# Performance work log

Measured on AMD Instinct MI355X. Metric: run time of the kernel, lower is better.

Reference implementation:

```python
import jax, jax.numpy as jnp
import numpy as np

OLD = (32, 32)   # fine grid coord_dims
NEW = (16, 16)   # coarse grid (dims // 2)
N_ORDERS = 6     # multi-indices of total order <= 2 in 2 coords


def lin_resize(x, new_size, axis):
    # 1D linear interpolation along `axis`, align_corners=True (matches F.interpolate)
    old = x.shape[axis]
    pos = jnp.arange(new_size, dtype=x.dtype) * ((old - 1) / (new_size - 1))
    lo = jnp.clip(jnp.floor(pos).astype(jnp.int32), 0, old - 2)
    w = pos - lo.astype(x.dtype)
    xl = jnp.take(x, lo, axis=axis)
    xh = jnp.take(x, lo + 1, axis=axis)
    shp = [1] * x.ndim
    shp[axis] = new_size
    w = w.reshape(shp)
    return xl * (1.0 - w) + xh * w


def bilinear_resize(x, new_hw):
    # separable bilinear, align_corners=True; x is [..., H, W]
    x = lin_resize(x, new_hw[0], x.ndim - 2)
    return lin_resize(x, new_hw[1], x.ndim - 1)


def setup_inputs():
    key = jax.random.key(0)
    ks = jax.random.split(key, 6)
    B = 32                      # bs * n_ind_dim = 8 * 4
    G = OLD[0] * OLD[1]         # fine grid size = 1024
    m, n = 2048, 1536           # coarse constraints x coarse vars (16*16*6)
    return {
        "coeffs": jax.random.normal(ks[0], (B, G, N_ORDERS), jnp.float32),
        "rhs": jax.random.normal(ks[1], (B, G), jnp.float32),
        "steps_x": jax.random.uniform(ks[2], (B, OLD[0] - 1), jnp.float32),
        "steps_y": jax.random.uniform(ks[3], (B, OLD[1] - 1), jnp.float32),
        "A": jax.random.normal(ks[4], (B, m, n), jnp.float32) * 0.05,
        "A_rhs": jax.random.normal(ks[5], (B, m), jnp.float32),
    }


def reference(coeffs, rhs, steps_x, steps_y, A, A_rhs):
    B = coeffs.shape[0]
    new_G = NEW[0] * NEW[1]

    # --- downsample_coeffs: [B,G,O] -> [B,O,H,W] -> bilinear -> [B,newG,O]
    c = coeffs.transpose(0, 2, 1).reshape(B, N_ORDERS, OLD[0], OLD[1])
    c = bilinear_resize(c, NEW)
    new_coeffs = c.reshape(B, N_ORDERS, new_G).transpose(0, 2, 1)

    # --- downsample_rhs: [B,G] -> [B,1,H,W] -> bilinear -> [B,newG]
    r = bilinear_resize(rhs.reshape(B, 1, OLD[0], OLD[1]), NEW)
    new_rhs = r.reshape(B, new_G)

    # --- downsample_steps: drop last, pairwise sum
    nsx = steps_x[:, :-1].reshape(B, OLD[0] // 2 - 1, 2).sum(axis=-1)
    nsy = steps_y[:, :-1].reshape(B, OLD[1] // 2 - 1, 2).sum(axis=-1)

    # --- make_AtA (coarsest path: dense bmm) ---
    AtA = jnp.einsum('bmn,bmk->bnk', A, A)           # At @ A, [B,n,n]
    AtPrhs = jnp.einsum('bmn,bm->bn', A, A_rhs)      # At @ rhs
    D = jnp.sum(A * A, axis=1)                       # diag(AtA) = column sums of squares

    # --- L/U split (get_tril): L = cols <= rows, U = cols > rows ---
    n = AtA.shape[-1]
    ridx = jnp.arange(n)
    lmask = ridx[:, None] >= ridx[None, :]
    L = jnp.where(lmask, AtA, jnp.zeros((), AtA.dtype))
    U = jnp.where(lmask, jnp.zeros((), AtA.dtype), AtA)

    return (new_coeffs, new_rhs, nsx, nsy, AtA, AtPrhs, D, L, U)
```

## Files before the change

### kernel.cpp

```cpp
#include <hip/hip_runtime.h>
#include <math.h>

#define NB 32
#define M 2048
#define N 1536
#define NORD 6

#define OFF_COEFFS 0
#define OFF_RHS    49152
#define OFF_NSX    57344
#define OFF_NSY    57824
#define OFF_ATA    58304
#define OFF_ATPRHS 75555776
#define OFF_D      75604928
#define OFF_L      75654080
#define OFF_U      151151552
#define SMALL_TOTAL 58304

typedef short short8v __attribute__((ext_vector_type(8)));
typedef float f32x4 __attribute__((ext_vector_type(4)));

__device__ __forceinline__ void gload16(const void* g, void* l) {
    __builtin_amdgcn_global_load_lds(
        (const __attribute__((address_space(1))) void*)g,
        (__attribute__((address_space(3))) void*)l, 16, 0, 0);
}

__device__ __forceinline__ uint rtn_bf16(float x) {
    uint u = __float_as_uint(x);
    return (u + 0x7fffu + ((u >> 16) & 1u)) >> 16;
}

__device__ __forceinline__ void nts(float v, float* p) {
    __builtin_nontemporal_store(v, p);
}
__device__ __forceinline__ void nts4(f32x4 v, float* p) {
    __builtin_nontemporal_store(v, (f32x4*)p);
}

__global__ void small_kernel(const float* __restrict__ coeffs,
                             const float* __restrict__ rhs,
                             const float* __restrict__ sx,
                             const float* __restrict__ sy,
                             float* __restrict__ out) {
    int idx = blockIdx.x * blockDim.x + threadIdx.x;
    if (idx >= SMALL_TOTAL) return;
    const float scale = 31.0f / 15.0f;
    if (idx < 49152) {
        int b = idx / 1536;
        int rem = idx % 1536;
        int gp = rem / 6;
        int o  = rem % 6;
        int yy = gp / 16, xx = gp % 16;
        float py = (float)yy * scale;
        int ly = (int)floorf(py); if (ly > 30) ly = 30;
        float wy = py - (float)ly;
        float px = (float)xx * scale;
        int lx = (int)floorf(px); if (lx > 30) lx = 30;
        float wx = px - (float)lx;
        const float* base = coeffs + (size_t)b * 1024 * NORD;
        float v00 = base[(ly * 32 + lx) * NORD + o];
        float v01 = base[(ly * 32 + lx + 1) * NORD + o];
        float v10 = base[((ly + 1) * 32 + lx) * NORD + o];
        float v11 = base[((ly + 1) * 32 + lx + 1) * NORD + o];
        float a  = v00 * (1.0f - wy) + v10 * wy;
        float bb = v01 * (1.0f - wy) + v11 * wy;
        out[OFF_COEFFS + idx] = a * (1.0f - wx) + bb * wx;
    } else if (idx < 57344) {
        int j = idx - 49152;
        int b = j / 256;
        int gp = j % 256;
        int yy = gp / 16, xx = gp % 16;
        float py = (float)yy * scale;
        int ly = (int)floorf(py); if (ly > 30) ly = 30;
        float wy = py - (float)ly;
        float px = (float)xx * scale;
        int lx = (int)floorf(px); if (lx > 30) lx = 30;
        float wx = px - (float)lx;
        const float* base = rhs + (size_t)b * 1024;
        float v00 = base[ly * 32 + lx];
        float v01 = base[ly * 32 + lx + 1];
        float v10 = base[(ly + 1) * 32 + lx];
        float v11 = base[(ly + 1) * 32 + lx + 1];
        float a  = v00 * (1.0f - wy) + v10 * wy;
        float bb = v01 * (1.0f - wy) + v11 * wy;
        out[OFF_RHS + j] = a * (1.0f - wx) + bb * wx;
    } else if (idx < 57824) {
        int j = idx - 57344;
        int b = j / 15, k = j % 15;
        out[OFF_NSX + j] = sx[b * 31 + 2 * k] + sx[b * 31 + 2 * k + 1];
    } else {
        int j = idx - 57824;
        int b = j / 15, k = j % 15;
        out[OFF_NSY + j] = sy[b * 31 + 2 * k] + sy[b * 31 + 2 * k + 1];
    }
}

__global__ __launch_bounds__(256) void split_kernel(const float* __restrict__ A,
                                                    const float* __restrict__ Arhs,
                                                    ushort* __restrict__ Ahi,
                                                    float2* __restrict__ part) {
    int bid = blockIdx.x;
    int q  = bid & 3;
    int cb = (bid >> 2) % 6;
    int b  = bid / 24;
    int t  = threadIdx.x;
    int col = cb * 256 + t;
    const float* Ab = A + (size_t)b * M * N;
    const float* rb = Arhs + (size_t)b * M;
    uint4* Hp = (uint4*)Ahi;
    float s1 = 0.0f, s2 = 0.0f;
    for (int oct = q * 64; oct < q * 64 + 64; ++oct) {
        uint hw[4];
#pragma unroll
        for (int j = 0; j < 4; ++j) {
            float a0 = Ab[(size_t)(oct * 8 + 2 * j) * N + col];
            float a1 = Ab[(size_t)(oct * 8 + 2 * j + 1) * N + col];
            float r0 = rb[oct * 8 + 2 * j];
            float r1 = rb[oct * 8 + 2 * j + 1];
            s1 = fmaf(a0, r0, s1); s1 = fmaf(a1, r1, s1);
            s2 = fmaf(a0, a0, s2); s2 = fmaf(a1, a1, s2);
            hw[j] = rtn_bf16(a0) | (rtn_bf16(a1) << 16);
        }
        Hp[(size_t)(b * 256 + oct) * N + col] = make_uint4(hw[0], hw[1], hw[2], hw[3]);
    }
    part[(size_t)q * (NB * 6 * 256) + (size_t)(b * 6 + cb) * 256 + t] = make_float2(s1, s2);
}

__global__ __launch_bounds__(256) void reduce_kernel(const float2* __restrict__ part,
                                                     float* __restrict__ out) {
    int idx = blockIdx.x * 256 + threadIdx.x;
    float s1 = 0.0f, s2 = 0.0f;
#pragma unroll
    for (int q = 0; q < 4; ++q) {
        float2 p = part[(size_t)q * (NB * 6 * 256) + idx];
        s1 += p.x; s2 += p.y;
    }
    out[OFF_ATPRHS + idx] = s1;
    out[OFF_D + idx] = s2;
}

#define SYRK_BLOCKS (NB * 42)

__global__ __launch_bounds__(512, 4) void syrk1_kernel(const ushort* __restrict__ Ahi,
                                                       float* __restrict__ out) {
    __shared__ ushort lds[2][1536 * 8];

    int bid = blockIdx.x;
    int swz = (bid % 8) * (SYRK_BLOCKS / 8) + bid / 8;
    int b  = swz / 42;
    int p2 = swz % 42;
    int p = p2 >> 1, half = p2 & 1;
    int ti = 0;
    while ((ti + 1) * (ti + 2) / 2 <= p) ++ti;
    int tj = p - ti * (ti + 1) / 2;
    bool diag = (ti == tj);
    int i0 = ti * 256;
    int j0 = tj * 256 + half * 128;

    int t = threadIdx.x, w = t >> 6, l = t & 63;
    int wr = w >> 1, wc = w & 1;
    int lc = l & 15, lg = l >> 4;

    const ushort* base = Ahi + (size_t)b * 256 * N * 8;

    f32x4 acc[4][4];
#pragma unroll
    for (int i = 0; i < 4; ++i)
#pragma unroll
        for (int j = 0; j < 4; ++j)
#pragma unroll
            for (int k = 0; k < 4; ++k) acc[i][j][k] = 0.0f;

    auto stage = [&](int buf, int s) {
#pragma unroll
        for (int q = 0; q < 2; ++q) {
            int g0 = q * 512 + w * 64;
            int oct = (g0 >> 8) & 3, col0 = g0 & 255;
            gload16(base + ((size_t)(s * 4 + oct) * N + i0 + col0 + l) * 8,
                    &lds[buf][(oct * 256 + col0) * 8]);
        }
        {
            int oct = w >> 1, col0 = (w & 1) * 64;
            gload16(base + ((size_t)(s * 4 + oct) * N + j0 + col0 + l) * 8,
                    &lds[buf][1024 * 8 + (oct * 128 + col0) * 8]);
        }
    };

    int cur = 0;
    stage(0, 0);

    for (int s = 0; s < 64; ++s) {
        if (s < 63) {
            stage(cur ^ 1, s + 1);
            asm volatile("s_waitcnt vmcnt(3)" ::: "memory");
        } else {
            asm volatile("s_waitcnt vmcnt(0)" ::: "memory");
        }
        __builtin_amdgcn_s_barrier();
        asm volatile("" ::: "memory");

        short8v Bv[4];
#pragma unroll
        for (int bj = 0; bj < 4; ++bj) {
            int cp = wc * 64 + bj * 16 + lc;
            Bv[bj] = *(const short8v*)&lds[cur][1024 * 8 + (lg * 128 + cp) * 8];
        }
        __builtin_amdgcn_s_setprio(1);
#pragma unroll
        for (int ai = 0; ai < 4; ++ai) {
            short8v Av = *(const short8v*)&lds[cur][(lg * 256 + wr * 64 + ai * 16 + lc) * 8];
#pragma unroll
            for (int bj = 0; bj < 4; ++bj)
                acc[ai][bj] = __builtin_amdgcn_mfma_f32_16x16x32_bf16(Av, Bv[bj], acc[ai][bj], 0, 0, 0);
        }
        __builtin_amdgcn_s_setprio(0);

        asm volatile("" ::: "memory");
        __builtin_amdgcn_s_barrier();
        cur ^= 1;
    }

    float* AtA = out + OFF_ATA + (size_t)b * N * N;
    float* Lo  = out + OFF_L   + (size_t)b * N * N;
    float* Up  = out + OFF_U   + (size_t)b * N * N;

#pragma unroll
    for (int ai = 0; ai < 4; ++ai) {
        int gi0 = i0 + wr * 64 + ai * 16 + lg * 4;
#pragma unroll
        for (int bj = 0; bj < 4; ++bj) {
            int gj = j0 + wc * 64 + bj * 16 + lc;
#pragma unroll
            for (int r = 0; r < 4; ++r) {
                int gi = gi0 + r;
                float v = acc[ai][bj][r];
                size_t o = (size_t)gi * N + gj;
                nts(v, AtA + o);
                nts((gj <= gi) ? v : 0.0f, Lo + o);
                nts((gj >  gi) ? v : 0.0f, Up + o);
            }
            if (!diag) {
                f32x4 va = acc[ai][bj], vl, vu;
#pragma unroll
                for (int r = 0; r < 4; ++r) {
                    int gi = gi0 + r;
                    vl[r] = (gi <= gj) ? va[r] : 0.0f;
                    vu[r] = (gi >  gj) ? va[r] : 0.0f;
                }
                size_t om = (size_t)gj * N + gi0;
                nts4(va, AtA + om);
                nts4(vl, Lo  + om);
                nts4(vu, Up  + om);
            }
        }
    }
}

__global__ __launch_bounds__(256) void atp_d_kernel(const float* __restrict__ A,
                                                    const float* __restrict__ Arhs,
                                                    float* __restrict__ out) {
    int b  = blockIdx.x / 6;
    int cb = blockIdx.x % 6;
    int col = cb * 256 + threadIdx.x;
    const float* Ab = A + (size_t)b * M * N;
    const float* rb = Arhs + (size_t)b * M;
    float s1 = 0.0f, s2 = 0.0f;
#pragma unroll 4
    for (int m = 0; m < M; ++m) {
        float a = Ab[(size_t)m * N + col];
        float r = rb[m];
        s1 = fmaf(a, r, s1);
        s2 = fmaf(a, a, s2);
    }
    out[OFF_ATPRHS + b * N + col] = s1;
    out[OFF_D      + b * N + col] = s2;
}

#define BM 128
#define BK 16
#define NPAIRS 78

__global__ __launch_bounds__(256, 2) void syrk_kernel(const float* __restrict__ A,
                                                      float* __restrict__ out) {
    __shared__ float As[BK][BM];
    __shared__ float Bs[BK][BM];

    int bid = blockIdx.x;
    int b = bid / NPAIRS;
    int p = bid % NPAIRS;
    int ti = (int)((sqrtf(8.0f * (float)p + 1.0f) - 1.0f) * 0.5f);
    while ((ti + 1) * (ti + 2) / 2 <= p) ++ti;
    while (ti * (ti + 1) / 2 > p) --ti;
    int tj = p - ti * (ti + 1) / 2;
    int i0 = ti * BM, j0 = tj * BM;

    const float* Ab = A + (size_t)b * M * N;
    int t = threadIdx.x;
    int tx = t % 16, ty = t / 16;
    int lcv = (t % 32) * 4;
    int lk = t / 32;

    float acc[2][4][2][4] = {};

    for (int m0 = 0; m0 < M; m0 += BK) {
        const float* pa = Ab + (size_t)(m0 + lk) * N;
        float4 a0 = *(const float4*)(pa + i0 + lcv);
        float4 a1 = *(const float4*)(pa + (size_t)8 * N + i0 + lcv);
        float4 b0 = *(const float4*)(pa + j0 + lcv);
        float4 b1 = *(const float4*)(pa + (size_t)8 * N + j0 + lcv);
        *(float4*)&As[lk][lcv]     = a0;
        *(float4*)&As[lk + 8][lcv] = a1;
        *(float4*)&Bs[lk][lcv]     = b0;
        *(float4*)&Bs[lk + 8][lcv] = b1;
        __syncthreads();
#pragma unroll
        for (int kk = 0; kk < BK; ++kk) {
            float ar[2][4], br[2][4];
            *(float4*)&ar[0][0] = *(const float4*)&As[kk][ty * 4];
            *(float4*)&ar[1][0] = *(const float4*)&As[kk][64 + ty * 4];
            *(float4*)&br[0][0] = *(const float4*)&Bs[kk][tx * 4];
            *(float4*)&br[1][0] = *(const float4*)&Bs[kk][64 + tx * 4];
#pragma unroll
            for (int rh = 0; rh < 2; ++rh)
#pragma unroll
                for (int r = 0; r < 4; ++r)
#pragma unroll
                    for (int ch = 0; ch < 2; ++ch)
#pragma unroll
                        for (int c = 0; c < 4; ++c)
                            acc[rh][r][ch][c] = fmaf(ar[rh][r], br[ch][c], acc[rh][r][ch][c]);
        }
        __syncthreads();
    }

    float* AtA = out + OFF_ATA + (size_t)b * N * N;
    float* L   = out + OFF_L   + (size_t)b * N * N;
    float* U   = out + OFF_U   + (size_t)b * N * N;

#pragma unroll
    for (int rh = 0; rh < 2; ++rh)
#pragma unroll
        for (int r = 0; r < 4; ++r) {
            int gi = i0 + rh * 64 + ty * 4 + r;
#pragma unroll
            for (int ch = 0; ch < 2; ++ch) {
                int gjb = j0 + ch * 64 + tx * 4;
                float ta[4], tl[4], tu[4];
#pragma unroll
                for (int c = 0; c < 4; ++c) {
                    int gj = gjb + c;
                    float v = acc[rh][r][ch][c];
                    ta[c] = v;
                    tl[c] = (gj <= gi) ? v : 0.0f;
                    tu[c] = (gj >  gi) ? v : 0.0f;
                }
                size_t o = (size_t)gi * N + gjb;
                *(float4*)(AtA + o) = *(float4*)ta;
                *(float4*)(L   + o) = *(float4*)tl;
                *(float4*)(U   + o) = *(float4*)tu;
            }
        }

    if (ti != tj) {
#pragma unroll
        for (int ch = 0; ch < 2; ++ch)
#pragma unroll
            for (int c = 0; c < 4; ++c) {
                int gj = j0 + ch * 64 + tx * 4 + c;
#pragma unroll
                for (int rh = 0; rh < 2; ++rh) {
                    int gib = i0 + rh * 64 + ty * 4;
                    float ta[4], tl[4], tu[4];
#pragma unroll
                    for (int r = 0; r < 4; ++r) {
                        int gi = gib + r;
                        float v = acc[rh][r][ch][c];
                        ta[r] = v;
                        tl[r] = (gi <= gj) ? v : 0.0f;
                        tu[r] = (gi >  gj) ? v : 0.0f;
                    }
                    size_t o = (size_t)gj * N + gib;
                    *(float4*)(AtA + o) = *(float4*)ta;
                    *(float4*)(L   + o) = *(float4*)tl;
                    *(float4*)(U   + o) = *(float4*)tu;
                }
            }
    }
}

extern "C" void kernel_launch(void* const* d_in, const int* in_sizes, int n_in,
                              void* d_out, int out_size, void* d_ws, size_t ws_size,
                              hipStream_t stream) {
    const float* coeffs = (const float*)d_in[0];
    const float* rhs    = (const float*)d_in[1];
    const float* sx     = (const float*)d_in[2];
    const float* sy     = (const float*)d_in[3];
    const float* A      = (const float*)d_in[4];
    const float* Arhs   = (const float*)d_in[5];
    float* out = (float*)d_out;

    small_kernel<<<(SMALL_TOTAL + 255) / 256, 256, 0, stream>>>(coeffs, rhs, sx, sy, out);

    const size_t hi_bytes   = (size_t)NB * M * N * sizeof(ushort);
    const size_t part_bytes = (size_t)4 * NB * 6 * 256 * sizeof(float2);
    if (ws_size >= hi_bytes + part_bytes) {
        ushort* Ahi  = (ushort*)d_ws;
        float2* part = (float2*)((char*)d_ws + hi_bytes);
        split_kernel<<<768, 256, 0, stream>>>(A, Arhs, Ahi, part);
        reduce_kernel<<<192, 256, 0, stream>>>(part, out);
        syrk1_kernel<<<SYRK_BLOCKS, 512, 0, stream>>>(Ahi, out);
    } else {
        atp_d_kernel<<<NB * 6, 256, 0, stream>>>(A, Arhs, out);
        syrk_kernel<<<NB * NPAIRS, 256, 0, stream>>>(A, out);
    }
}
```

Before: 519.8 us.

## Use 256x256 SYRK tiles with deeper multi-stage LDS pipeline

```diff
diff --git a/kernel.cpp b/kernel.cpp
--- a/kernel.cpp
+++ b/kernel.cpp
@@ -140,85 +140,108 @@
     out[OFF_D + idx] = s2;
 }
 
-#define SYRK_BLOCKS (NB * 42)
-
-__global__ __launch_bounds__(512, 4) void syrk1_kernel(const ushort* __restrict__ Ahi,
+#define SYRK8_BLOCKS (NB * 21)
+
+__global__ __launch_bounds__(512, 2) void syrk8_kernel(const ushort* __restrict__ Ahi,
                                                        float* __restrict__ out) {
-    __shared__ ushort lds[2][1536 * 8];
+    __shared__ ushort lds[2][2][8 * 256 * 8];
 
     int bid = blockIdx.x;
-    int swz = (bid % 8) * (SYRK_BLOCKS / 8) + bid / 8;
-    int b  = swz / 42;
-    int p2 = swz % 42;
-    int p = p2 >> 1, half = p2 & 1;
+    int swz = (bid % 8) * (SYRK8_BLOCKS / 8) + bid / 8;
+    int b  = swz / 21;
+    int pp = swz % 21;
     int ti = 0;
-    while ((ti + 1) * (ti + 2) / 2 <= p) ++ti;
-    int tj = p - ti * (ti + 1) / 2;
+    while ((ti + 1) * (ti + 2) / 2 <= pp) ++ti;
+    int tj = pp - ti * (ti + 1) / 2;
     bool diag = (ti == tj);
-    int i0 = ti * 256;
-    int j0 = tj * 256 + half * 128;
+    int i0 = ti * 256, j0 = tj * 256;
 
     int t = threadIdx.x, w = t >> 6, l = t & 63;
-    int wr = w >> 1, wc = w & 1;
+    int wr = w >> 2, wc = w & 3;
     int lc = l & 15, lg = l >> 4;
 
     const ushort* base = Ahi + (size_t)b * 256 * N * 8;
 
-    f32x4 acc[4][4];
-#pragma unroll
-    for (int i = 0; i < 4; ++i)
+    f32x4 acc[8][4];
+#pragma unroll
+    for (int i = 0; i < 8; ++i)
 #pragma unroll
         for (int j = 0; j < 4; ++j)
 #pragma unroll
             for (int k = 0; k < 4; ++k) acc[i][j][k] = 0.0f;
 
-    auto stage = [&](int buf, int s) {
-#pragma unroll
-        for (int q = 0; q < 2; ++q) {
-            int g0 = q * 512 + w * 64;
-            int oct = (g0 >> 8) & 3, col0 = g0 & 255;
-            gload16(base + ((size_t)(s * 4 + oct) * N + i0 + col0 + l) * 8,
-                    &lds[buf][(oct * 256 + col0) * 8]);
-        }
-        {
-            int oct = w >> 1, col0 = (w & 1) * 64;
-            gload16(base + ((size_t)(s * 4 + oct) * N + j0 + col0 + l) * 8,
-                    &lds[buf][1024 * 8 + (oct * 128 + col0) * 8]);
+    int oc0 = t >> 8;
+    int scol = t & 255;
+    auto stage_unit = [&](int n) {
+        int kt = n >> 2, u = n & 3;
+        int arr = u & 1, h = u >> 1;
+        int colb = arr ? j0 : i0;
+        ushort* reg = &lds[kt & 1][arr][0];
+#pragma unroll
+        for (int c = 0; c < 2; ++c) {
+            int oct = h * 4 + c * 2 + oc0;
+            gload16(base + ((size_t)(kt * 8 + oct) * N + colb + scol) * 8,
+                    reg + (size_t)(oct * 256 + scol) * 8);
         }
     };
 
-    int cur = 0;
-    stage(0, 0);
-
-    for (int s = 0; s < 64; ++s) {
-        if (s < 63) {
-            stage(cur ^ 1, s + 1);
-            asm volatile("s_waitcnt vmcnt(3)" ::: "memory");
-        } else {
-            asm volatile("s_waitcnt vmcnt(0)" ::: "memory");
-        }
-        __builtin_amdgcn_s_barrier();
-        asm volatile("" ::: "memory");
-
+    for (int n = 0; n < 8; ++n) stage_unit(n);
+    asm volatile("s_waitcnt vmcnt(12)" ::: "memory");
+    __builtin_amdgcn_s_barrier();
+
+    for (int it = 0; it < 16; ++it) {
         short8v Bv[4];
 #pragma unroll
-        for (int bj = 0; bj < 4; ++bj) {
-            int cp = wc * 64 + bj * 16 + lc;
-            Bv[bj] = *(const short8v*)&lds[cur][1024 * 8 + (lg * 128 + cp) * 8];
-        }
-        __builtin_amdgcn_s_setprio(1);
-#pragma unroll
-        for (int ai = 0; ai < 4; ++ai) {
-            short8v Av = *(const short8v*)&lds[cur][(lg * 256 + wr * 64 + ai * 16 + lc) * 8];
-#pragma unroll
-            for (int bj = 0; bj < 4; ++bj)
-                acc[ai][bj] = __builtin_amdgcn_mfma_f32_16x16x32_bf16(Av, Bv[bj], acc[ai][bj], 0, 0, 0);
-        }
-        __builtin_amdgcn_s_setprio(0);
-
-        asm volatile("" ::: "memory");
-        __builtin_amdgcn_s_barrier();
-        cur ^= 1;
+        for (int p = 0; p < 8; ++p) {
+            const int buf  = p >> 2;
+            const int ksub = (p >> 1) & 1;
+            const int ch   = p & 1;
+            const ushort* Areg = &lds[buf][0][0];
+            const ushort* Breg = &lds[buf][1][0];
+
+            short8v Av[4];
+#pragma unroll
+            for (int aif = 0; aif < 4; ++aif) {
+                int ai = ch * 4 + aif;
+                Av[aif] = *(const short8v*)
+                    &Areg[(size_t)((ksub * 4 + lg) * 256 + wr * 128 + ai * 16 + lc) * 8];
+            }
+            if (ch == 0) {
+#pragma unroll
+                for (int bj = 0; bj < 4; ++bj)
+                    Bv[bj] = *(const short8v*)
+                        &Breg[(size_t)((ksub * 4 + lg) * 256 + wc * 64 + bj * 16 + lc) * 8];
+            }
+
+            int g = it * 8 + p;
+            if (g >= 2 && g <= 121) stage_unit(g + 6);
+
+            asm volatile("" ::: "memory");
+            __builtin_amdgcn_s_barrier();
+            asm volatile("s_waitcnt lgkmcnt(0)" ::: "memory");
+            __builtin_amdgcn_sched_barrier(0);
+
+            __builtin_amdgcn_s_setprio(1);
+#pragma unroll
+            for (int aif = 0; aif < 4; ++aif)
+#pragma unroll
+                for (int bj = 0; bj < 4; ++bj)
+                    acc[ch * 4 + aif][bj] = __builtin_amdgcn_mfma_f32_16x16x32_bf16(
+                        Av[aif], Bv[bj], acc[ch * 4 + aif][bj], 0, 0, 0);
+            __builtin_amdgcn_s_setprio(0);
+
+            if (p == 1) {
+                if (it == 15) asm volatile("s_waitcnt vmcnt(4)" ::: "memory");
+                else          asm volatile("s_waitcnt vmcnt(8)" ::: "memory");
+            } else if (p == 3 || p == 5) {
+                if (it == 15) asm volatile("s_waitcnt vmcnt(0)" ::: "memory");
+                else          asm volatile("s_waitcnt vmcnt(8)" ::: "memory");
+            } else if (p == 7) {
+                if (it != 15) asm volatile("s_waitcnt vmcnt(8)" ::: "memory");
+            }
+            asm volatile("" ::: "memory");
+            __builtin_amdgcn_s_barrier();
+        }
     }
 
     float* AtA = out + OFF_ATA + (size_t)b * N * N;
@@ -226,8 +249,8 @@
     float* Up  = out + OFF_U   + (size_t)b * N * N;
 
 #pragma unroll
-    for (int ai = 0; ai < 4; ++ai) {
-        int gi0 = i0 + wr * 64 + ai * 16 + lg * 4;
+    for (int ai = 0; ai < 8; ++ai) {
+        int gi0 = i0 + wr * 128 + ai * 16 + lg * 4;
 #pragma unroll
         for (int bj = 0; bj < 4; ++bj) {
             int gj = j0 + wc * 64 + bj * 16 + lc;
@@ -409,7 +432,7 @@
         float2* part = (float2*)((char*)d_ws + hi_bytes);
         split_kernel<<<768, 256, 0, stream>>>(A, Arhs, Ahi, part);
         reduce_kernel<<<192, 256, 0, stream>>>(part, out);
-        syrk1_kernel<<<SYRK_BLOCKS, 512, 0, stream>>>(Ahi, out);
+        syrk8_kernel<<<SYRK8_BLOCKS, 512, 0, stream>>>(Ahi, out);
     } else {
         atp_d_kernel<<<NB * 6, 256, 0, stream>>>(A, Arhs, out);
         syrk_kernel<<<NB * NPAIRS, 256, 0, stream>>>(A, out);
```

Result: slower. 531.9 us (+2.3%).

## Use 128x128 SYRK tiles with 256-thread blocks and shared diagonal operand

Applied to the files above, without the earlier changes.

```diff
diff --git a/kernel.cpp b/kernel.cpp
--- a/kernel.cpp
+++ b/kernel.cpp
@@ -140,23 +140,21 @@
     out[OFF_D + idx] = s2;
 }
 
-#define SYRK_BLOCKS (NB * 42)
-
-__global__ __launch_bounds__(512, 4) void syrk1_kernel(const ushort* __restrict__ Ahi,
+#define SYRK_BLOCKS (NB * 78)
+
+__global__ __launch_bounds__(256, 4) void syrk3_kernel(const ushort* __restrict__ Ahi,
                                                        float* __restrict__ out) {
-    __shared__ ushort lds[2][1536 * 8];
+    __shared__ ushort lds[2][1024 * 8];
 
     int bid = blockIdx.x;
     int swz = (bid % 8) * (SYRK_BLOCKS / 8) + bid / 8;
-    int b  = swz / 42;
-    int p2 = swz % 42;
-    int p = p2 >> 1, half = p2 & 1;
+    int b = swz / 78;
+    int p = swz % 78;
     int ti = 0;
     while ((ti + 1) * (ti + 2) / 2 <= p) ++ti;
     int tj = p - ti * (ti + 1) / 2;
     bool diag = (ti == tj);
-    int i0 = ti * 256;
-    int j0 = tj * 256 + half * 128;
+    int i0 = ti * 128, j0 = tj * 128;
 
     int t = threadIdx.x, w = t >> 6, l = t & 63;
     int wr = w >> 1, wc = w & 1;
@@ -172,44 +170,45 @@
 #pragma unroll
             for (int k = 0; k < 4; ++k) acc[i][j][k] = 0.0f;
 
+    int nq = diag ? 2 : 4;
     auto stage = [&](int buf, int s) {
-#pragma unroll
-        for (int q = 0; q < 2; ++q) {
-            int g0 = q * 512 + w * 64;
-            int oct = (g0 >> 8) & 3, col0 = g0 & 255;
-            gload16(base + ((size_t)(s * 4 + oct) * N + i0 + col0 + l) * 8,
-                    &lds[buf][(oct * 256 + col0) * 8]);
-        }
-        {
-            int oct = w >> 1, col0 = (w & 1) * 64;
-            gload16(base + ((size_t)(s * 4 + oct) * N + j0 + col0 + l) * 8,
-                    &lds[buf][1024 * 8 + (oct * 128 + col0) * 8]);
+        ushort* Lb = &lds[buf][0];
+#pragma unroll
+        for (int q = 0; q < 4; ++q) {
+            if (q < nq) {
+                int G = q * 256 + t;
+                int arr = G >> 9, oct = (G >> 7) & 3, col = G & 127;
+                int colb = arr ? j0 : i0;
+                gload16(base + ((size_t)(s * 4 + oct) * N + colb + col) * 8,
+                        &Lb[(size_t)G * 8]);
+            }
         }
     };
 
+    stage(0, 0);
+
     int cur = 0;
-    stage(0, 0);
-
     for (int s = 0; s < 64; ++s) {
         if (s < 63) {
             stage(cur ^ 1, s + 1);
-            asm volatile("s_waitcnt vmcnt(3)" ::: "memory");
+            if (diag) asm volatile("s_waitcnt vmcnt(2)" ::: "memory");
+            else      asm volatile("s_waitcnt vmcnt(4)" ::: "memory");
         } else {
             asm volatile("s_waitcnt vmcnt(0)" ::: "memory");
         }
         __builtin_amdgcn_s_barrier();
         asm volatile("" ::: "memory");
 
+        const ushort* Areg = &lds[cur][0];
+        const ushort* Breg = diag ? Areg : (Areg + 512 * 8);
         short8v Bv[4];
 #pragma unroll
-        for (int bj = 0; bj < 4; ++bj) {
-            int cp = wc * 64 + bj * 16 + lc;
-            Bv[bj] = *(const short8v*)&lds[cur][1024 * 8 + (lg * 128 + cp) * 8];
-        }
+        for (int bj = 0; bj < 4; ++bj)
+            Bv[bj] = *(const short8v*)&Breg[(size_t)(lg * 128 + wc * 64 + bj * 16 + lc) * 8];
         __builtin_amdgcn_s_setprio(1);
 #pragma unroll
         for (int ai = 0; ai < 4; ++ai) {
-            short8v Av = *(const short8v*)&lds[cur][(lg * 256 + wr * 64 + ai * 16 + lc) * 8];
+            short8v Av = *(const short8v*)&Areg[(size_t)(lg * 128 + wr * 64 + ai * 16 + lc) * 8];
 #pragma unroll
             for (int bj = 0; bj < 4; ++bj)
                 acc[ai][bj] = __builtin_amdgcn_mfma_f32_16x16x32_bf16(Av, Bv[bj], acc[ai][bj], 0, 0, 0);
@@ -409,7 +408,7 @@
         float2* part = (float2*)((char*)d_ws + hi_bytes);
         split_kernel<<<768, 256, 0, stream>>>(A, Arhs, Ahi, part);
         reduce_kernel<<<192, 256, 0, stream>>>(part, out);
-        syrk1_kernel<<<SYRK_BLOCKS, 512, 0, stream>>>(Ahi, out);
+        syrk3_kernel<<<SYRK_BLOCKS, 256, 0, stream>>>(Ahi, out);
     } else {
         atp_d_kernel<<<NB * 6, 256, 0, stream>>>(A, Arhs, out);
         syrk_kernel<<<NB * NPAIRS, 256, 0, stream>>>(A, out);
```

Result: slower. 550.9 us (+6.0%).
